# Kernel tuning notes

Hardware: AMD Instinct MI355X
Metric: run time of the kernel (lower is better)

The kernel has to match this reference:

```python
import jax, jax.numpy as jnp
import numpy as np

NUM_GRAPHS = 64


def _gcn_conv(x, src, dst, W, b, num_nodes):
    """PyG GCNConv: h = D^-1/2 (A+I) D^-1/2 (x W) + b (self-loops already in src/dst)."""
    h = x @ W  # [N, out]
    deg = jax.ops.segment_sum(jnp.ones_like(src, dtype=h.dtype), dst, num_segments=num_nodes)
    dinv = jnp.where(deg > 0, jax.lax.rsqrt(jnp.maximum(deg, 1e-12)), 0.0)
    norm = dinv[src] * dinv[dst]  # [E+N]
    msg = h[src] * norm[:, None]  # gather + scale
    out = jax.ops.segment_sum(msg, dst, num_segments=num_nodes)  # scatter-add
    return out + b


def setup_inputs() -> dict:
    key = jax.random.key(0)
    k1, k2, k3, k4, k5, k6, k7, k8, k9 = jax.random.split(key, 9)
    N, E, D_IN, D_H, D_OUT = 50000, 800000, 128, 64, 7
    x = jax.random.normal(k1, (N, D_IN), dtype=jnp.float32)
    edge_index = jax.random.randint(k2, (2, E), 0, N, dtype=jnp.int64)
    batch = jnp.sort(jax.random.randint(k3, (N,), 0, NUM_GRAPHS, dtype=jnp.int64))
    s = 1.0 / np.sqrt(D_IN)
    W1 = jax.random.uniform(k4, (D_IN, D_H), minval=-s, maxval=s, dtype=jnp.float32)
    b1 = jnp.zeros((D_H,), jnp.float32)
    s2 = 1.0 / np.sqrt(D_H)
    W2 = jax.random.uniform(k5, (D_H, D_H), minval=-s2, maxval=s2, dtype=jnp.float32)
    b2 = jnp.zeros((D_H,), jnp.float32)
    s3 = 1.0 / np.sqrt(2 * D_H)
    Wlin = jax.random.uniform(k6, (2 * D_H, D_OUT), minval=-s3, maxval=s3, dtype=jnp.float32)
    blin = jax.random.uniform(k7, (D_OUT,), minval=-s3, maxval=s3, dtype=jnp.float32)
    return {"x": x, "edge_index": edge_index, "batch": batch,
            "W1": W1, "b1": b1, "W2": W2, "b2": b2, "Wlin": Wlin, "blin": blin}


def reference(x, edge_index, batch, W1, b1, W2, b2, Wlin, blin):
    N = x.shape[0]
    loops = jnp.arange(N, dtype=edge_index.dtype)
    src = jnp.concatenate([edge_index[0], loops])
    dst = jnp.concatenate([edge_index[1], loops])
    # dropout is identity in eval mode
    x1 = jax.nn.relu(_gcn_conv(x, src, dst, W1, b1, N))
    x2 = jax.nn.relu(_gcn_conv(x1, src, dst, W2, b2, N))
    xc = jnp.concatenate([x1, x2], axis=-1)  # JumpingKnowledge 'cat' -> [N, 128]
    summed = jax.ops.segment_sum(xc, batch, num_segments=NUM_GRAPHS)
    counts = jax.ops.segment_sum(jnp.ones((N,), xc.dtype), batch, num_segments=NUM_GRAPHS)
    pooled = summed / jnp.maximum(counts, 1.0)[:, None]  # global mean pool [G, 128]
    return pooled @ Wlin + blin  # [G, output_size]
```

## Files before the change

### kernel.cpp

```cpp
#include <hip/hip_runtime.h>

static constexpr int NUM_GRAPHS = 64;
static constexpr int DH = 64;
static constexpr int DOUT = 7;
static constexpr int EPB = 8192;
static constexpr int BSH = 8;

__global__ __launch_bounds__(256) void hist_kernel(const int* __restrict__ ei,
                                                   int* __restrict__ hist,
                                                   int E, int NBLK, int NBUCK) {
    __shared__ int lh[256];
    int t = threadIdx.x, blk = blockIdx.x;
    lh[t] = 0;
    __syncthreads();
    int s = blk * EPB, e = min(E, s + EPB);
    for (int i = s + t; i < e; i += 256)
        atomicAdd(&lh[ei[E + i] >> BSH], 1);
    __syncthreads();
    if (t < NBUCK) hist[t * NBLK + blk] = lh[t];
}

__global__ __launch_bounds__(256) void partial_kernel(const int* __restrict__ in,
                                                      int* __restrict__ bsum, int L) {
    __shared__ int sh[256];
    int t = threadIdx.x;
    int i = blockIdx.x * 256 + t;
    sh[t] = (i < L) ? in[i] : 0;
    __syncthreads();
    for (int s = 128; s > 0; s >>= 1) {
        if (t < s) sh[t] += sh[t + s];
        __syncthreads();
    }
    if (t == 0) bsum[blockIdx.x] = sh[0];
}

__global__ __launch_bounds__(256) void escan_kernel(const int* __restrict__ in,
                                                    const int* __restrict__ bsum,
                                                    int* __restrict__ offs, int L) {
    __shared__ int red[256];
    __shared__ int sh[256];
    int t = threadIdx.x, b = blockIdx.x, i = b * 256 + t;
    int part = 0;
    for (int j = t; j < b; j += 256) part += bsum[j];
    red[t] = part;
    __syncthreads();
    for (int s = 128; s > 0; s >>= 1) {
        if (t < s) red[t] += red[t + s];
        __syncthreads();
    }
    int base = red[0];
    int d = (i < L) ? in[i] : 0;
    sh[t] = d;
    __syncthreads();
    for (int off = 1; off < 256; off <<= 1) {
        int v = (t >= off) ? sh[t - off] : 0;
        __syncthreads();
        sh[t] += v;
        __syncthreads();
    }
    if (i < L) offs[i] = base + sh[t] - d;
}

__global__ __launch_bounds__(256) void scatter_kernel(const int* __restrict__ ei,
                                                      const int* __restrict__ offs,
                                                      int2* __restrict__ ebuf,
                                                      int E, int NBLK, int NBUCK) {
    __shared__ int cur[256];
    int t = threadIdx.x, blk = blockIdx.x;
    if (t < NBUCK) cur[t] = offs[t * NBLK + blk];
    __syncthreads();
    int s = blk * EPB, e = min(E, s + EPB);
    for (int i = s + t; i < e; i += 256) {
        int src = ei[i], dst = ei[E + i];
        int p = atomicAdd(&cur[dst >> BSH], 1);
        ebuf[p] = make_int2(src, dst);
    }
}

__global__ __launch_bounds__(256) void brow_kernel(const int2* __restrict__ ebuf,
                                                   const int* __restrict__ offs,
                                                   int* __restrict__ rowptr,
                                                   float* __restrict__ dinv,
                                                   int N, int E, int NBLK, int NBUCK) {
    __shared__ int dcnt[256];
    __shared__ int sc[256];
    int t = threadIdx.x, B = blockIdx.x;
    dcnt[t] = 0;
    __syncthreads();
    int beg = offs[B * NBLK];
    int end = (B + 1 < NBUCK) ? offs[(B + 1) * NBLK] : E;
    for (int i = beg + t; i < end; i += 256)
        atomicAdd(&dcnt[ebuf[i].y & 255], 1);
    __syncthreads();
    int v = B * 256 + t;
    int d = (v < N) ? dcnt[t] + 1 : 0;
    sc[t] = d;
    __syncthreads();
    for (int off = 1; off < 256; off <<= 1) {
        int vv = (t >= off) ? sc[t - off] : 0;
        __syncthreads();
        sc[t] += vv;
        __syncthreads();
    }
    int base = beg + B * 256;
    if (v < N) {
        rowptr[v] = base + sc[t] - d;
        dinv[v] = rsqrtf((float)(dcnt[t] + 1));
    }
    if (B == 0 && t == 0) rowptr[N] = E + N;
}

__global__ __launch_bounds__(256) void bfill_kernel(const int2* __restrict__ ebuf,
                                                    const int* __restrict__ offs,
                                                    const int* __restrict__ rowptr,
                                                    const float* __restrict__ dinv,
                                                    int2* __restrict__ csr,
                                                    int N, int E, int NBLK, int NBUCK) {
    __shared__ int cur[256];
    __shared__ float sdv[256];
    int t = threadIdx.x, B = blockIdx.x;
    int v = B * 256 + t;
    if (v < N) {
        int p = rowptr[v];
        float dv = dinv[v];
        csr[p] = make_int2(v, __float_as_int(dv * dv));
        cur[t] = p + 1;
        sdv[t] = dv;
    } else {
        cur[t] = 0;
        sdv[t] = 0.f;
    }
    __syncthreads();
    int beg = offs[B * NBLK];
    int end = (B + 1 < NBUCK) ? offs[(B + 1) * NBLK] : E;
    for (int i = beg + t; i < end; i += 256) {
        int2 ed = ebuf[i];
        int l = ed.y & 255;
        int p = atomicAdd(&cur[l], 1);
        csr[p] = make_int2(ed.x, __float_as_int(dinv[ed.x] * sdv[l]));
    }
}

template <int K>
__global__ __launch_bounds__(256) void gemm_kernel(const float* __restrict__ x,
                                                   const float* __restrict__ W,
                                                   float* __restrict__ h, int N) {
    __shared__ float4 sX4[64][K / 4];
    __shared__ float  sW[K][64];
    int t = threadIdx.x;
    int r0 = blockIdx.x * 64;

    const float4* W4 = (const float4*)W;
    for (int v = t; v < K * 16; v += 256) {
        int k = v >> 4, c4 = v & 15;
        *(float4*)&sW[k][c4 * 4] = W4[v];
    }
    for (int v = t; v < 64 * (K / 4); v += 256) {
        int row = v / (K / 4), c4 = v % (K / 4);
        int gr = min(r0 + row, N - 1);
        sX4[row][c4] = *(const float4*)(x + (size_t)gr * K + 4 * c4);
    }
    __syncthreads();

    int c = t & 63;
    int w = t >> 6;
    float acc[16];
#pragma unroll
    for (int r = 0; r < 16; ++r) acc[r] = 0.f;

#pragma unroll 2
    for (int k4 = 0; k4 < K / 4; ++k4) {
        float w0 = sW[4 * k4 + 0][c];
        float w1 = sW[4 * k4 + 1][c];
        float w2 = sW[4 * k4 + 2][c];
        float w3 = sW[4 * k4 + 3][c];
#pragma unroll
        for (int r = 0; r < 16; ++r) {
            float4 xv = sX4[w * 16 + r][k4];
            acc[r] = fmaf(xv.x, w0, acc[r]);
            acc[r] = fmaf(xv.y, w1, acc[r]);
            acc[r] = fmaf(xv.z, w2, acc[r]);
            acc[r] = fmaf(xv.w, w3, acc[r]);
        }
    }

#pragma unroll
    for (int r = 0; r < 16; ++r) {
        int row = r0 + w * 16 + r;
        if (row < N) h[(size_t)row * DH + c] = acc[r];
    }
}

__global__ __launch_bounds__(256) void agg_kernel(const float* __restrict__ h,
                                                  const int2* __restrict__ csr,
                                                  const int* __restrict__ rowptr,
                                                  const float* __restrict__ bias,
                                                  float* __restrict__ out, int N) {
    int lane = threadIdx.x & 63;
    int node = blockIdx.x * (blockDim.x >> 6) + (threadIdx.x >> 6);
    if (node >= N) return;
    int g = lane >> 4;
    int s = lane & 15;

    float4 acc0 = {0.f, 0.f, 0.f, 0.f};
    float4 acc1 = {0.f, 0.f, 0.f, 0.f};
    float4 acc2 = {0.f, 0.f, 0.f, 0.f};
    float4 acc3 = {0.f, 0.f, 0.f, 0.f};
    int beg = rowptr[node], end = rowptr[node + 1];
    int i = beg;
    for (; i + 16 <= end; i += 16) {
        int2 ea = csr[i + g];
        int2 eb = csr[i + 4 + g];
        int2 ec = csr[i + 8 + g];
        int2 ed = csr[i + 12 + g];
        float4 ha = ((const float4*)(h + (size_t)ea.x * DH))[s];
        float4 hb = ((const float4*)(h + (size_t)eb.x * DH))[s];
        float4 hc = ((const float4*)(h + (size_t)ec.x * DH))[s];
        float4 hd = ((const float4*)(h + (size_t)ed.x * DH))[s];
        float wa = __int_as_float(ea.y), wb = __int_as_float(eb.y);
        float wc = __int_as_float(ec.y), wd = __int_as_float(ed.y);
        acc0.x = fmaf(wa, ha.x, acc0.x); acc0.y = fmaf(wa, ha.y, acc0.y);
        acc0.z = fmaf(wa, ha.z, acc0.z); acc0.w = fmaf(wa, ha.w, acc0.w);
        acc1.x = fmaf(wb, hb.x, acc1.x); acc1.y = fmaf(wb, hb.y, acc1.y);
        acc1.z = fmaf(wb, hb.z, acc1.z); acc1.w = fmaf(wb, hb.w, acc1.w);
        acc2.x = fmaf(wc, hc.x, acc2.x); acc2.y = fmaf(wc, hc.y, acc2.y);
        acc2.z = fmaf(wc, hc.z, acc2.z); acc2.w = fmaf(wc, hc.w, acc2.w);
        acc3.x = fmaf(wd, hd.x, acc3.x); acc3.y = fmaf(wd, hd.y, acc3.y);
        acc3.z = fmaf(wd, hd.z, acc3.z); acc3.w = fmaf(wd, hd.w, acc3.w);
    }
    for (; i + 8 <= end; i += 8) {
        int2 ea = csr[i + g];
        int2 eb = csr[i + 4 + g];
        float4 ha = ((const float4*)(h + (size_t)ea.x * DH))[s];
        float4 hb = ((const float4*)(h + (size_t)eb.x * DH))[s];
        float wa = __int_as_float(ea.y), wb = __int_as_float(eb.y);
        acc0.x = fmaf(wa, ha.x, acc0.x); acc0.y = fmaf(wa, ha.y, acc0.y);
        acc0.z = fmaf(wa, ha.z, acc0.z); acc0.w = fmaf(wa, ha.w, acc0.w);
        acc1.x = fmaf(wb, hb.x, acc1.x); acc1.y = fmaf(wb, hb.y, acc1.y);
        acc1.z = fmaf(wb, hb.z, acc1.z); acc1.w = fmaf(wb, hb.w, acc1.w);
    }
    if (i + 4 <= end) {
        int2 ea = csr[i + g];
        float4 ha = ((const float4*)(h + (size_t)ea.x * DH))[s];
        float wa = __int_as_float(ea.y);
        acc0.x = fmaf(wa, ha.x, acc0.x); acc0.y = fmaf(wa, ha.y, acc0.y);
        acc0.z = fmaf(wa, ha.z, acc0.z); acc0.w = fmaf(wa, ha.w, acc0.w);
        i += 4;
    }
    if (i + g < end) {
        int2 ea = csr[i + g];
        float4 ha = ((const float4*)(h + (size_t)ea.x * DH))[s];
        float wa = __int_as_float(ea.y);
        acc2.x = fmaf(wa, ha.x, acc2.x); acc2.y = fmaf(wa, ha.y, acc2.y);
        acc2.z = fmaf(wa, ha.z, acc2.z); acc2.w = fmaf(wa, ha.w, acc2.w);
    }
    float4 acc;
    acc.x = (acc0.x + acc1.x) + (acc2.x + acc3.x);
    acc.y = (acc0.y + acc1.y) + (acc2.y + acc3.y);
    acc.z = (acc0.z + acc1.z) + (acc2.z + acc3.z);
    acc.w = (acc0.w + acc1.w) + (acc2.w + acc3.w);

    acc.x += __shfl_xor(acc.x, 16); acc.y += __shfl_xor(acc.y, 16);
    acc.z += __shfl_xor(acc.z, 16); acc.w += __shfl_xor(acc.w, 16);
    acc.x += __shfl_xor(acc.x, 32); acc.y += __shfl_xor(acc.y, 32);
    acc.z += __shfl_xor(acc.z, 32); acc.w += __shfl_xor(acc.w, 32);

    if (g == 0) {
        float4 bv = ((const float4*)bias)[s];
        float4 o;
        o.x = fmaxf(acc.x + bv.x, 0.f);
        o.y = fmaxf(acc.y + bv.y, 0.f);
        o.z = fmaxf(acc.z + bv.z, 0.f);
        o.w = fmaxf(acc.w + bv.w, 0.f);
        ((float4*)(out + (size_t)node * DH))[s] = o;
    }
}

__global__ __launch_bounds__(128) void pool_kernel(const float* __restrict__ x1,
                                                   const float* __restrict__ x2,
                                                   const int* __restrict__ batch,
                                                   float* __restrict__ pool,
                                                   float* __restrict__ cntf,
                                                   int N, int nodesPerBlock) {
    int f = threadIdx.x;
    int start = blockIdx.x * nodesPerBlock;
    int end = min(N, start + nodesPerBlock);
    if (start >= end) return;
    int gcur = batch[start];
    float acc = 0.f;
    int c = 0;
    for (int v = start; v < end; ++v) {
        int g = batch[v];
        if (g != gcur) {
            atomicAdd(&pool[gcur * 128 + f], acc);
            if (f == 0) atomicAdd(&cntf[gcur], (float)c);
            acc = 0.f; c = 0; gcur = g;
        }
        acc += (f < DH) ? x1[(size_t)v * DH + f] : x2[(size_t)v * DH + (f - DH)];
        ++c;
    }
    atomicAdd(&pool[gcur * 128 + f], acc);
    if (f == 0) atomicAdd(&cntf[gcur], (float)c);
}

__global__ __launch_bounds__(512) void final_kernel(const float* __restrict__ pool,
                                                    const float* __restrict__ cntf,
                                                    const float* __restrict__ Wlin,
                                                    const float* __restrict__ blin,
                                                    float* __restrict__ out) {
    int t = threadIdx.x;
    if (t >= NUM_GRAPHS * DOUT) return;
    int g = t / DOUT, o = t % DOUT;
    float inv = 1.0f / fmaxf(cntf[g], 1.0f);
    float acc = 0.f;
    for (int k = 0; k < 2 * DH; ++k)
        acc = fmaf(pool[g * 128 + k], Wlin[k * DOUT + o], acc);
    out[t] = acc * inv + blin[o];
}

extern "C" void kernel_launch(void* const* d_in, const int* in_sizes, int n_in,
                              void* d_out, int out_size, void* d_ws, size_t ws_size,
                              hipStream_t stream) {
    const float* x    = (const float*)d_in[0];
    const int*   ei   = (const int*)d_in[1];
    const int*   batch= (const int*)d_in[2];
    const float* W1   = (const float*)d_in[3];
    const float* b1   = (const float*)d_in[4];
    const float* W2   = (const float*)d_in[5];
    const float* b2   = (const float*)d_in[6];
    const float* Wlin = (const float*)d_in[7];
    const float* blin = (const float*)d_in[8];
    float* out = (float*)d_out;

    const int N = in_sizes[2];
    const int E = in_sizes[1] / 2;
    const int DIN = in_sizes[0] / N;
    const int NBUCK = (N + 255) >> BSH;
    const int NBLK = (E + EPB - 1) / EPB;
    const int L = NBUCK * NBLK;
    const int LB = (L + 255) / 256;

    char* base = (char*)d_ws;
    size_t off = 0;
    auto alloc = [&](size_t bytes) {
        char* p = base + off;
        off = (off + bytes + 255) & ~(size_t)255;
        return p;
    };
    int*   hist   = (int*)  alloc((size_t)L * 4);
    int*   offs   = (int*)  alloc((size_t)L * 4);
    int*   bsum   = (int*)  alloc((size_t)LB * 4);
    int*   rowptr = (int*)  alloc((size_t)(N + 1) * 4);
    float* dinv   = (float*)alloc((size_t)N * 4);
    int2*  ebuf   = (int2*) alloc((size_t)E * 8);
    int2*  csr    = (int2*) alloc((size_t)(E + N) * 8);
    float* h      = (float*)alloc((size_t)N * DH * 4);
    float* x1     = (float*)alloc((size_t)N * DH * 4);
    float* x2     = (float*)alloc((size_t)N * DH * 4);
    float* pool   = (float*)alloc((size_t)NUM_GRAPHS * 128 * 4);
    float* cntf   = (float*)alloc((size_t)NUM_GRAPHS * 4);
    (void)ws_size; (void)n_in; (void)out_size; (void)DIN;

    hipMemsetAsync(pool, 0, (size_t)NUM_GRAPHS * 128 * 4, stream);
    hipMemsetAsync(cntf, 0, (size_t)NUM_GRAPHS * 4, stream);

    hist_kernel<<<NBLK, 256, 0, stream>>>(ei, hist, E, NBLK, NBUCK);
    partial_kernel<<<LB, 256, 0, stream>>>(hist, bsum, L);
    escan_kernel<<<LB, 256, 0, stream>>>(hist, bsum, offs, L);
    scatter_kernel<<<NBLK, 256, 0, stream>>>(ei, offs, ebuf, E, NBLK, NBUCK);
    brow_kernel<<<NBUCK, 256, 0, stream>>>(ebuf, offs, rowptr, dinv, N, E, NBLK, NBUCK);
    bfill_kernel<<<NBUCK, 256, 0, stream>>>(ebuf, offs, rowptr, dinv, csr, N, E, NBLK, NBUCK);

    gemm_kernel<128><<<(N + 63) / 64, 256, 0, stream>>>(x, W1, h, N);
    agg_kernel<<<(N + 3) / 4, 256, 0, stream>>>(h, csr, rowptr, b1, x1, N);
    gemm_kernel<64><<<(N + 63) / 64, 256, 0, stream>>>(x1, W2, h, N);
    agg_kernel<<<(N + 3) / 4, 256, 0, stream>>>(h, csr, rowptr, b2, x2, N);

    const int nodesPerBlock = 32;
    pool_kernel<<<(N + nodesPerBlock - 1) / nodesPerBlock, 128, 0, stream>>>(
        x1, x2, batch, pool, cntf, N, nodesPerBlock);
    final_kernel<<<1, 512, 0, stream>>>(pool, cntf, Wlin, blin, out);
}
```

Before: 276.8 us.

## Factor GCN normalization into GEMM and aggregation; pack CSR as int indices

The symmetric D^-1/2 normalization is split so the GEMM output is pre-scaled by dinv[src] and the aggregation applies dinv[dst] once per node. The CSR then only needs source indices, which halves edge-list traffic in the gather loop. The edge buffer packs src and the local dst into one int, and the row-pointer and fill kernels are merged so bucket edges are staged in LDS and read from global memory once. The packing assumes src fits in 24 bits, and the change adds a 32KB LDS array that may lower occupancy of the build kernel.

```diff
diff --git a/kernel.cpp b/kernel.cpp
--- a/kernel.cpp
+++ b/kernel.cpp
@@ -5,6 +5,8 @@
 static constexpr int DOUT = 7;
 static constexpr int EPB = 8192;
 static constexpr int BSH = 8;
+static constexpr int LDSCAP = 8192;
+
 
 __global__ __launch_bounds__(256) void hist_kernel(const int* __restrict__ ei,
                                                    int* __restrict__ hist,
@@ -63,7 +65,7 @@
 
 __global__ __launch_bounds__(256) void scatter_kernel(const int* __restrict__ ei,
                                                       const int* __restrict__ offs,
-                                                      int2* __restrict__ ebuf,
+                                                      int* __restrict__ ebuf,
                                                       int E, int NBLK, int NBUCK) {
     __shared__ int cur[256];
     int t = threadIdx.x, blk = blockIdx.x;
@@ -73,25 +75,40 @@
     for (int i = s + t; i < e; i += 256) {
         int src = ei[i], dst = ei[E + i];
         int p = atomicAdd(&cur[dst >> BSH], 1);
-        ebuf[p] = make_int2(src, dst);
-    }
-}
-
-__global__ __launch_bounds__(256) void brow_kernel(const int2* __restrict__ ebuf,
-                                                   const int* __restrict__ offs,
-                                                   int* __restrict__ rowptr,
-                                                   float* __restrict__ dinv,
-                                                   int N, int E, int NBLK, int NBUCK) {
+        ebuf[p] = (src << BSH) | (dst & 255);
+    }
+}
+
+__global__ __launch_bounds__(256) void browfill_kernel(const int* __restrict__ ebuf,
+                                                       const int* __restrict__ offs,
+                                                       int* __restrict__ rowptr,
+                                                       float* __restrict__ dinv,
+                                                       int* __restrict__ csr,
+                                                       int N, int E, int NBLK, int NBUCK) {
+    __shared__ int eld[LDSCAP];
     __shared__ int dcnt[256];
     __shared__ int sc[256];
+    __shared__ int cur[256];
     int t = threadIdx.x, B = blockIdx.x;
-    dcnt[t] = 0;
-    __syncthreads();
     int beg = offs[B * NBLK];
     int end = (B + 1 < NBUCK) ? offs[(B + 1) * NBLK] : E;
-    for (int i = beg + t; i < end; i += 256)
-        atomicAdd(&dcnt[ebuf[i].y & 255], 1);
-    __syncthreads();
+    int cnt = end - beg;
+    bool inlds = (cnt <= LDSCAP);
+
+    dcnt[t] = 0;
+    __syncthreads();
+    if (inlds) {
+        for (int i = t; i < cnt; i += 256) {
+            int p = ebuf[beg + i];
+            eld[i] = p;
+            atomicAdd(&dcnt[p & 255], 1);
+        }
+    } else {
+        for (int i = t; i < cnt; i += 256)
+            atomicAdd(&dcnt[ebuf[beg + i] & 255], 1);
+    }
+    __syncthreads();
+
     int v = B * 256 + t;
     int d = (v < N) ? dcnt[t] + 1 : 0;
     sc[t] = d;
@@ -104,46 +121,36 @@
     }
     int base = beg + B * 256;
     if (v < N) {
-        rowptr[v] = base + sc[t] - d;
+        int rp = base + sc[t] - d;
+        rowptr[v] = rp;
         dinv[v] = rsqrtf((float)(dcnt[t] + 1));
-    }
-    if (B == 0 && t == 0) rowptr[N] = E + N;
-}
-
-__global__ __launch_bounds__(256) void bfill_kernel(const int2* __restrict__ ebuf,
-                                                    const int* __restrict__ offs,
-                                                    const int* __restrict__ rowptr,
-                                                    const float* __restrict__ dinv,
-                                                    int2* __restrict__ csr,
-                                                    int N, int E, int NBLK, int NBUCK) {
-    __shared__ int cur[256];
-    __shared__ float sdv[256];
-    int t = threadIdx.x, B = blockIdx.x;
-    int v = B * 256 + t;
-    if (v < N) {
-        int p = rowptr[v];
-        float dv = dinv[v];
-        csr[p] = make_int2(v, __float_as_int(dv * dv));
-        cur[t] = p + 1;
-        sdv[t] = dv;
+        csr[rp] = v;
+        cur[t] = rp + 1;
     } else {
         cur[t] = 0;
-        sdv[t] = 0.f;
-    }
-    __syncthreads();
-    int beg = offs[B * NBLK];
-    int end = (B + 1 < NBUCK) ? offs[(B + 1) * NBLK] : E;
-    for (int i = beg + t; i < end; i += 256) {
-        int2 ed = ebuf[i];
-        int l = ed.y & 255;
-        int p = atomicAdd(&cur[l], 1);
-        csr[p] = make_int2(ed.x, __float_as_int(dinv[ed.x] * sdv[l]));
+    }
+    if (B == 0 && t == 0) rowptr[N] = E + N;
+    __syncthreads();
+
+    if (inlds) {
+        for (int i = t; i < cnt; i += 256) {
+            int p = eld[i];
+            int pos = atomicAdd(&cur[p & 255], 1);
+            csr[pos] = p >> BSH;
+        }
+    } else {
+        for (int i = t; i < cnt; i += 256) {
+            int p = ebuf[beg + i];
+            int pos = atomicAdd(&cur[p & 255], 1);
+            csr[pos] = p >> BSH;
+        }
     }
 }
 
 template <int K>
 __global__ __launch_bounds__(256) void gemm_kernel(const float* __restrict__ x,
                                                    const float* __restrict__ W,
+                                                   const float* __restrict__ dinv,
                                                    float* __restrict__ h, int N) {
     __shared__ float4 sX4[64][K / 4];
     __shared__ float  sW[K][64];
@@ -187,13 +194,14 @@
 #pragma unroll
     for (int r = 0; r < 16; ++r) {
         int row = r0 + w * 16 + r;
-        if (row < N) h[(size_t)row * DH + c] = acc[r];
+        if (row < N) h[(size_t)row * DH + c] = acc[r] * dinv[row];
     }
 }
 
 __global__ __launch_bounds__(256) void agg_kernel(const float* __restrict__ h,
-                                                  const int2* __restrict__ csr,
+                                                  const int* __restrict__ csr,
                                                   const int* __restrict__ rowptr,
+                                                  const float* __restrict__ dinv,
                                                   const float* __restrict__ bias,
                                                   float* __restrict__ out, int N) {
     int lane = threadIdx.x & 63;
@@ -209,50 +217,37 @@
     int beg = rowptr[node], end = rowptr[node + 1];
     int i = beg;
     for (; i + 16 <= end; i += 16) {
-        int2 ea = csr[i + g];
-        int2 eb = csr[i + 4 + g];
-        int2 ec = csr[i + 8 + g];
-        int2 ed = csr[i + 12 + g];
-        float4 ha = ((const float4*)(h + (size_t)ea.x * DH))[s];
-        float4 hb = ((const float4*)(h + (size_t)eb.x * DH))[s];
-        float4 hc = ((const float4*)(h + (size_t)ec.x * DH))[s];
-        float4 hd = ((const float4*)(h + (size_t)ed.x * DH))[s];
-        float wa = __int_as_float(ea.y), wb = __int_as_float(eb.y);
-        float wc = __int_as_float(ec.y), wd = __int_as_float(ed.y);
-        acc0.x = fmaf(wa, ha.x, acc0.x); acc0.y = fmaf(wa, ha.y, acc0.y);
-        acc0.z = fmaf(wa, ha.z, acc0.z); acc0.w = fmaf(wa, ha.w, acc0.w);
-        acc1.x = fmaf(wb, hb.x, acc1.x); acc1.y = fmaf(wb, hb.y, acc1.y);
-        acc1.z = fmaf(wb, hb.z, acc1.z); acc1.w = fmaf(wb, hb.w, acc1.w);
-        acc2.x = fmaf(wc, hc.x, acc2.x); acc2.y = fmaf(wc, hc.y, acc2.y);
-        acc2.z = fmaf(wc, hc.z, acc2.z); acc2.w = fmaf(wc, hc.w, acc2.w);
-        acc3.x = fmaf(wd, hd.x, acc3.x); acc3.y = fmaf(wd, hd.y, acc3.y);
-        acc3.z = fmaf(wd, hd.z, acc3.z); acc3.w = fmaf(wd, hd.w, acc3.w);
+        int sa = csr[i + g];
+        int sb = csr[i + 4 + g];
+        int sc_ = csr[i + 8 + g];
+        int sd = csr[i + 12 + g];
+        float4 ha = ((const float4*)(h + (size_t)sa * DH))[s];
+        float4 hb = ((const float4*)(h + (size_t)sb * DH))[s];
+        float4 hc = ((const float4*)(h + (size_t)sc_ * DH))[s];
+        float4 hd = ((const float4*)(h + (size_t)sd * DH))[s];
+        acc0.x += ha.x; acc0.y += ha.y; acc0.z += ha.z; acc0.w += ha.w;
+        acc1.x += hb.x; acc1.y += hb.y; acc1.z += hb.z; acc1.w += hb.w;
+        acc2.x += hc.x; acc2.y += hc.y; acc2.z += hc.z; acc2.w += hc.w;
+        acc3.x += hd.x; acc3.y += hd.y; acc3.z += hd.z; acc3.w += hd.w;
     }
     for (; i + 8 <= end; i += 8) {
-        int2 ea = csr[i + g];
-        int2 eb = csr[i + 4 + g];
-        float4 ha = ((const float4*)(h + (size_t)ea.x * DH))[s];
-        float4 hb = ((const float4*)(h + (size_t)eb.x * DH))[s];
-        float wa = __int_as_float(ea.y), wb = __int_as_float(eb.y);
-        acc0.x = fmaf(wa, ha.x, acc0.x); acc0.y = fmaf(wa, ha.y, acc0.y);
-        acc0.z = fmaf(wa, ha.z, acc0.z); acc0.w = fmaf(wa, ha.w, acc0.w);
-        acc1.x = fmaf(wb, hb.x, acc1.x); acc1.y = fmaf(wb, hb.y, acc1.y);
-        acc1.z = fmaf(wb, hb.z, acc1.z); acc1.w = fmaf(wb, hb.w, acc1.w);
+        int sa = csr[i + g];
+        int sb = csr[i + 4 + g];
+        float4 ha = ((const float4*)(h + (size_t)sa * DH))[s];
+        float4 hb = ((const float4*)(h + (size_t)sb * DH))[s];
+        acc0.x += ha.x; acc0.y += ha.y; acc0.z += ha.z; acc0.w += ha.w;
+        acc1.x += hb.x; acc1.y += hb.y; acc1.z += hb.z; acc1.w += hb.w;
     }
     if (i + 4 <= end) {
-        int2 ea = csr[i + g];
-        float4 ha = ((const float4*)(h + (size_t)ea.x * DH))[s];
-        float wa = __int_as_float(ea.y);
-        acc0.x = fmaf(wa, ha.x, acc0.x); acc0.y = fmaf(wa, ha.y, acc0.y);
-        acc0.z = fmaf(wa, ha.z, acc0.z); acc0.w = fmaf(wa, ha.w, acc0.w);
+        int sa = csr[i + g];
+        float4 ha = ((const float4*)(h + (size_t)sa * DH))[s];
+        acc0.x += ha.x; acc0.y += ha.y; acc0.z += ha.z; acc0.w += ha.w;
         i += 4;
     }
     if (i + g < end) {
-        int2 ea = csr[i + g];
-        float4 ha = ((const float4*)(h + (size_t)ea.x * DH))[s];
-        float wa = __int_as_float(ea.y);
-        acc2.x = fmaf(wa, ha.x, acc2.x); acc2.y = fmaf(wa, ha.y, acc2.y);
-        acc2.z = fmaf(wa, ha.z, acc2.z); acc2.w = fmaf(wa, ha.w, acc2.w);
+        int sa = csr[i + g];
+        float4 ha = ((const float4*)(h + (size_t)sa * DH))[s];
+        acc2.x += ha.x; acc2.y += ha.y; acc2.z += ha.z; acc2.w += ha.w;
     }
     float4 acc;
     acc.x = (acc0.x + acc1.x) + (acc2.x + acc3.x);
@@ -266,12 +261,13 @@
     acc.z += __shfl_xor(acc.z, 32); acc.w += __shfl_xor(acc.w, 32);
 
     if (g == 0) {
+        float dv = dinv[node];
         float4 bv = ((const float4*)bias)[s];
         float4 o;
-        o.x = fmaxf(acc.x + bv.x, 0.f);
-        o.y = fmaxf(acc.y + bv.y, 0.f);
-        o.z = fmaxf(acc.z + bv.z, 0.f);
-        o.w = fmaxf(acc.w + bv.w, 0.f);
+        o.x = fmaxf(fmaf(dv, acc.x, bv.x), 0.f);
+        o.y = fmaxf(fmaf(dv, acc.y, bv.y), 0.f);
+        o.z = fmaxf(fmaf(dv, acc.z, bv.z), 0.f);
+        o.w = fmaxf(fmaf(dv, acc.w, bv.w), 0.f);
         ((float4*)(out + (size_t)node * DH))[s] = o;
     }
 }
@@ -352,8 +348,8 @@
     int*   bsum   = (int*)  alloc((size_t)LB * 4);
     int*   rowptr = (int*)  alloc((size_t)(N + 1) * 4);
     float* dinv   = (float*)alloc((size_t)N * 4);
-    int2*  ebuf   = (int2*) alloc((size_t)E * 8);
-    int2*  csr    = (int2*) alloc((size_t)(E + N) * 8);
+    int*   ebuf   = (int*)  alloc((size_t)E * 4);
+    int*   csr    = (int*)  alloc((size_t)(E + N) * 4);
     float* h      = (float*)alloc((size_t)N * DH * 4);
     float* x1     = (float*)alloc((size_t)N * DH * 4);
     float* x2     = (float*)alloc((size_t)N * DH * 4);
@@ -361,20 +357,18 @@
     float* cntf   = (float*)alloc((size_t)NUM_GRAPHS * 4);
     (void)ws_size; (void)n_in; (void)out_size; (void)DIN;
 
-    hipMemsetAsync(pool, 0, (size_t)NUM_GRAPHS * 128 * 4, stream);
-    hipMemsetAsync(cntf, 0, (size_t)NUM_GRAPHS * 4, stream);
+    hipMemsetAsync(pool, 0, (size_t)NUM_GRAPHS * 128 * 4 + (size_t)NUM_GRAPHS * 4, stream);
 
     hist_kernel<<<NBLK, 256, 0, stream>>>(ei, hist, E, NBLK, NBUCK);
     partial_kernel<<<LB, 256, 0, stream>>>(hist, bsum, L);
     escan_kernel<<<LB, 256, 0, stream>>>(hist, bsum, offs, L);
     scatter_kernel<<<NBLK, 256, 0, stream>>>(ei, offs, ebuf, E, NBLK, NBUCK);
-    brow_kernel<<<NBUCK, 256, 0, stream>>>(ebuf, offs, rowptr, dinv, N, E, NBLK, NBUCK);
-    bfill_kernel<<<NBUCK, 256, 0, stream>>>(ebuf, offs, rowptr, dinv, csr, N, E, NBLK, NBUCK);
-
-    gemm_kernel<128><<<(N + 63) / 64, 256, 0, stream>>>(x, W1, h, N);
-    agg_kernel<<<(N + 3) / 4, 256, 0, stream>>>(h, csr, rowptr, b1, x1, N);
-    gemm_kernel<64><<<(N + 63) / 64, 256, 0, stream>>>(x1, W2, h, N);
-    agg_kernel<<<(N + 3) / 4, 256, 0, stream>>>(h, csr, rowptr, b2, x2, N);
+    browfill_kernel<<<NBUCK, 256, 0, stream>>>(ebuf, offs, rowptr, dinv, csr, N, E, NBLK, NBUCK);
+
+    gemm_kernel<128><<<(N + 63) / 64, 256, 0, stream>>>(x, W1, dinv, h, N);
+    agg_kernel<<<(N + 3) / 4, 256, 0, stream>>>(h, csr, rowptr, dinv, b1, x1, N);
+    gemm_kernel<64><<<(N + 63) / 64, 256, 0, stream>>>(x1, W2, dinv, h, N);
+    agg_kernel<<<(N + 3) / 4, 256, 0, stream>>>(h, csr, rowptr, dinv, b2, x2, N);
 
     const int nodesPerBlock = 32;
     pool_kernel<<<(N + nodesPerBlock - 1) / nodesPerBlock, 128, 0, stream>>>(
```

Measured after the change: 271.6 us. About the same (-1.9%).
